# Kernel optimization log

Measured on AMD Instinct MI355X. Metric: run time of the kernel, lower is better.

The kernel has to match this reference:

```python
import jax, jax.numpy as jnp
import numpy as np

B, S, D = 2, 2048, 1024
H, KV, HD = 16, 8, 64
E, K, FF = 8, 2, 3584
EPS = 1e-5
THETA = 10000.0


def setup_inputs() -> dict:
    key = jax.random.key(0)
    ks = jax.random.split(key, 10)
    sc = 0.02
    return {
        "hidden_states": jax.random.normal(ks[0], (B, S, D), jnp.float32),
        "position_ids": jnp.broadcast_to(jnp.arange(S, dtype=jnp.int32), (B, S)),
        "lb_loss": jnp.zeros((), jnp.float32),
        "ln1_w": jnp.ones((D,), jnp.float32),
        "ln2_w": jnp.ones((D,), jnp.float32),
        "Wq": jax.random.normal(ks[1], (D, H * HD), jnp.float32) * sc,
        "Wk": jax.random.normal(ks[2], (D, KV * HD), jnp.float32) * sc,
        "Wv": jax.random.normal(ks[3], (D, KV * HD), jnp.float32) * sc,
        "Wo": jax.random.normal(ks[4], (H * HD, D), jnp.float32) * sc,
        "Wg": jax.random.normal(ks[5], (D, E), jnp.float32) * sc,
        "w1": jax.random.normal(ks[6], (E, D, FF), jnp.float32) * sc,
        "w2": jax.random.normal(ks[7], (E, FF, D), jnp.float32) * sc,
        "w3": jax.random.normal(ks[8], (E, D, FF), jnp.float32) * sc,
    }


def rmsnorm(x, w):
    xf = x.astype(jnp.float32)
    return (w * (xf * jax.lax.rsqrt(jnp.mean(xf * xf, -1, keepdims=True) + EPS))).astype(x.dtype)


def rotate_half(x):
    x1, x2 = jnp.split(x, 2, axis=-1)
    return jnp.concatenate([-x2, x1], axis=-1)


def _forward(hidden_states, position_ids, lb_loss, ln1_w, ln2_w, Wq, Wk, Wv, Wo, Wg, w1, w2, w3):
    # ---- attention block (pre-norm + causal GQA + RoPE + residual) ----
    resid = hidden_states
    x = rmsnorm(hidden_states, ln1_w)
    q = (x @ Wq).reshape(B, S, H, HD)
    k = (x @ Wk).reshape(B, S, KV, HD)
    v = (x @ Wv).reshape(B, S, KV, HD)
    inv_freq = 1.0 / (THETA ** (jnp.arange(0, HD, 2, dtype=jnp.float32) / HD))
    ang = position_ids.astype(jnp.float32)[:, :, None] * inv_freq      # [B,S,HD/2]
    emb = jnp.concatenate([ang, ang], axis=-1)                          # [B,S,HD]
    cos = jnp.cos(emb)[:, :, None, :]
    sin = jnp.sin(emb)[:, :, None, :]
    q = q * cos + rotate_half(q) * sin
    k = k * cos + rotate_half(k) * sin
    rep = H // KV
    k = jnp.repeat(k, rep, axis=2)                                      # [B,S,H,HD]
    v = jnp.repeat(v, rep, axis=2)
    scores = jnp.einsum('bqhd,bkhd->bhqk', q, k) / jnp.sqrt(jnp.float32(HD))
    causal = jnp.tril(jnp.ones((S, S), bool))
    scores = jnp.where(causal[None, None], scores, jnp.float32(-1e30))
    probs = jax.nn.softmax(scores.astype(jnp.float32), axis=-1).astype(q.dtype)
    attn = jnp.einsum('bhqk,bkhd->bqhd', probs, v).reshape(B, S, H * HD)
    hidden_states = resid + attn @ Wo

    # ---- MoE block (pre-norm + top-2 routed SwiGLU experts + residual) ----
    resid = hidden_states
    x = rmsnorm(hidden_states, ln2_w)
    flat = x.reshape(-1, D)                                             # [N,D]
    logits = flat @ Wg
    gate_probs = jax.nn.softmax(logits.astype(jnp.float32), axis=-1)    # [N,E]
    top_w, top_i = jax.lax.top_k(gate_probs, K)                         # [N,K]
    top_w = (top_w / jnp.sum(top_w, -1, keepdims=True)).astype(flat.dtype)
    out = jnp.zeros_like(flat)
    for e in range(E):  # fixed small expert count
        w_e = jnp.sum(jnp.where(top_i == e, top_w, 0.0), axis=-1)       # [N]
        y = (jax.nn.silu(flat @ w1[e]) * (flat @ w3[e])) @ w2[e]        # [N,D]
        out = out + y * w_e[:, None]
    hidden_states = resid + out.reshape(B, S, D)

    # ---- load-balancing auxiliary loss ----
    expert_mask = jax.nn.one_hot(top_i, E, dtype=jnp.float32)           # [N,K,E]
    tokens_per_expert = jnp.mean(expert_mask, axis=0)                   # [K,E]
    router_prob_per_expert = jnp.mean(gate_probs, axis=0)               # [E]
    lb = jnp.mean(jnp.sum(tokens_per_expert * router_prob_per_expert[None, :], axis=-1)) * E
    return hidden_states, lb_loss + lb


def reference(hidden_states, position_ids, lb_loss, ln1_w, ln2_w, Wq, Wk, Wv, Wo, Wg, w1, w2, w3):
    return _forward(hidden_states, position_ids, lb_loss, ln1_w, ln2_w, Wq, Wk, Wv, Wo, Wg, w1, w2, w3)
```

## Files before the change

### kernel.cpp

```cpp
#include <hip/hip_runtime.h>
#include <stdint.h>

#define DEV __device__ __forceinline__

typedef __attribute__((ext_vector_type(8))) short short8;
typedef __attribute__((ext_vector_type(4))) float f32x4;
typedef __attribute__((ext_vector_type(4))) short short4v;

static constexpr int BATCH = 2, SEQ = 2048, DM = 1024, NH = 16, NKV = 8, HD = 64;
static constexpr int NTOK = BATCH * SEQ;
static constexpr int NE = 8, FF = 3584;

DEV unsigned short f2bf(float f) {
  union { float f; unsigned u; } x; x.f = f;
  unsigned r = x.u + 0x7fffu + ((x.u >> 16) & 1u);
  return (unsigned short)(r >> 16);
}
DEV float bf2f(unsigned short h) {
  union { unsigned u; float f; } x; x.u = ((unsigned)h) << 16; return x.f;
}

DEV void async16(const void* g, void* l) {
  __builtin_amdgcn_global_load_lds((const __attribute__((address_space(1))) unsigned int*)g,
                                   (__attribute__((address_space(3))) unsigned int*)l, 16, 0, 0);
}

DEV f32x4 mfma16(short8 a, short8 b, f32x4 c) {
  return __builtin_amdgcn_mfma_f32_16x16x32_bf16(a, b, c, 0, 0, 0);
}

__global__ __launch_bounds__(256) void transpose_cvt_k(
    const float* __restrict__ in, unsigned short* __restrict__ out,
    int R, int C, long inStride, long outStride)
{
  __shared__ unsigned short tile[64][68];
  const float* src = in + (long)blockIdx.z * inStride;
  unsigned short* dst = out + (long)blockIdx.z * outStride;
  int r0 = blockIdx.y * 64, c0 = blockIdx.x * 64;
  int s4 = (threadIdx.x & 15) * 4, rr = threadIdx.x >> 4;
#pragma unroll
  for (int i = 0; i < 4; ++i) {
    int r = rr + i * 16;
    float4 v = *(const float4*)(src + (long)(r0 + r) * C + c0 + s4);
    tile[r][s4 + 0] = f2bf(v.x); tile[r][s4 + 1] = f2bf(v.y);
    tile[r][s4 + 2] = f2bf(v.z); tile[r][s4 + 3] = f2bf(v.w);
  }
  __syncthreads();
#pragma unroll
  for (int i = 0; i < 4; ++i) {
    int c = rr + i * 16;
    union { unsigned short us[4]; short4v v; } o;
    o.us[0] = tile[s4 + 0][c]; o.us[1] = tile[s4 + 1][c];
    o.us[2] = tile[s4 + 2][c]; o.us[3] = tile[s4 + 3][c];
    *(short4v*)(dst + (long)(c0 + c) * R + r0 + s4) = o.v;
  }
}

__global__ __launch_bounds__(256) void rmsnorm_k(
    const float* __restrict__ x, const float* __restrict__ w, unsigned short* __restrict__ out)
{
  int row = blockIdx.x, t = threadIdx.x;
  const float4* xr = (const float4*)(x + (long)row * DM);
  float4 v = xr[t];
  float ss = v.x * v.x + v.y * v.y + v.z * v.z + v.w * v.w;
#pragma unroll
  for (int o = 32; o; o >>= 1) ss += __shfl_xor(ss, o);
  __shared__ float red[4];
  if ((t & 63) == 0) red[t >> 6] = ss;
  __syncthreads();
  float tot = red[0] + red[1] + red[2] + red[3];
  float rms = rsqrtf(tot * (1.0f / DM) + 1e-5f);
  float4 wv = ((const float4*)w)[t];
  union { unsigned short us[4]; short4v s; } o4;
  o4.us[0] = f2bf(v.x * rms * wv.x);
  o4.us[1] = f2bf(v.y * rms * wv.y);
  o4.us[2] = f2bf(v.z * rms * wv.z);
  o4.us[3] = f2bf(v.w * rms * wv.w);
  *(short4v*)(out + (long)row * DM + 4 * t) = o4.s;
}

template<int MODE>
__global__ __launch_bounds__(256) void gemm_k(
    const unsigned short* __restrict__ A, const unsigned short* __restrict__ B0,
    void* __restrict__ Cout, const float* __restrict__ resid,
    int M, int N, int K, int ldA, int ldB, int ldC)
{
  constexpr int BM = 128, BN = 128, BK = 64;
  __shared__ __align__(16) unsigned short As[BM * BK];
  __shared__ __align__(16) unsigned short Bs[BN * BK];
  int bm = blockIdx.x, bn = blockIdx.y;
  int t = threadIdx.x, w = t >> 6, l = t & 63, g = l >> 4, q = l & 15;
  int wm = w >> 1, wn = w & 1;

  const char* aSrc[4];
  const char* bSrc[4];
#pragma unroll
  for (int i = 0; i < 4; ++i) {
    int r = i * 32 + w * 8 + (l >> 3);
    aSrc[i] = (const char*)(A + (long)(bm * BM + r) * ldA) + (((l & 7) * 16) ^ ((r & 7) << 4));
    bSrc[i] = (const char*)(B0 + (long)(bn * BN + r) * ldB) + (((l & 7) * 16) ^ ((r & 7) << 4));
  }
  f32x4 acc[4][4];
#pragma unroll
  for (int mi = 0; mi < 4; ++mi)
#pragma unroll
    for (int ni = 0; ni < 4; ++ni) acc[mi][ni] = f32x4{0.f, 0.f, 0.f, 0.f};

  for (int k0 = 0; k0 < K; k0 += BK) {
#pragma unroll
    for (int i = 0; i < 4; ++i) {
      async16(aSrc[i] + (long)k0 * 2, &As[(i * 32 + w * 8) * BK]);
      async16(bSrc[i] + (long)k0 * 2, &Bs[(i * 32 + w * 8) * BK]);
    }
    asm volatile("s_waitcnt vmcnt(0)" ::: "memory");
    __syncthreads();
#pragma unroll
    for (int kk = 0; kk < 2; ++kk) {
      int col = (kk * 64 + g * 16) ^ ((q & 7) << 4);
      short8 af[4], bfm[4];
#pragma unroll
      for (int mi = 0; mi < 4; ++mi)
        af[mi] = *(const short8*)&As[(wm * 64 + mi * 16 + q) * BK + (col >> 1)];
#pragma unroll
      for (int ni = 0; ni < 4; ++ni)
        bfm[ni] = *(const short8*)&Bs[(wn * 64 + ni * 16 + q) * BK + (col >> 1)];
#pragma unroll
      for (int mi = 0; mi < 4; ++mi)
#pragma unroll
        for (int ni = 0; ni < 4; ++ni)
          acc[mi][ni] = mfma16(af[mi], bfm[ni], acc[mi][ni]);
    }
    __syncthreads();
  }
#pragma unroll
  for (int mi = 0; mi < 4; ++mi) {
#pragma unroll
    for (int r = 0; r < 4; ++r) {
      int grow = bm * BM + wm * 64 + mi * 16 + g * 4 + r;
#pragma unroll
      for (int ni = 0; ni < 4; ++ni) {
        int gcol = bn * BN + wn * 64 + ni * 16 + q;
        float v = acc[mi][ni][r];
        if (MODE == 0) {
          ((unsigned short*)Cout)[(long)grow * ldC + gcol] = f2bf(v);
        } else {
          long idx = (long)grow * ldC + gcol;
          ((float*)Cout)[idx] = resid[idx] + v;
        }
      }
    }
  }
}

__global__ __launch_bounds__(256, 3) void moe_up_k(
    const unsigned short* __restrict__ xn, const unsigned short* __restrict__ w1T,
    const unsigned short* __restrict__ w3T, unsigned short* __restrict__ hbuf,
    const int* __restrict__ lstAll, const int* __restrict__ cntAll)
{
  constexpr int BM = 128, BN = 64, BK = 64, NBN = FF / BN;
  constexpr int NJJ = NBN / 8;
  __shared__ __align__(16) unsigned short As[BM * BK];
  __shared__ __align__(16) unsigned short Bs[2][BN * BK];
  int t = threadIdx.x, w = t >> 6, l = t & 63, g = l >> 4, q = l & 15;
  int wm = w >> 1, wn = w & 1;
  int xcd = blockIdx.x & 7, slot = blockIdx.x >> 3, SLOTS = gridDim.x >> 3;

  int TB = 0;
#pragma unroll
  for (int e = 0; e < NE; ++e) TB += (cntAll[e] + BM - 1) >> 7;

  for (int lidx = slot; lidx < NJJ * TB; lidx += SLOTS) {
    int jj = lidx / TB, tb = lidx - jj * TB;
    int bn = xcd + 8 * jj;
    int e = 0, base = 0, cnt = 0, bm = 0;
    for (; e < NE; ++e) {
      cnt = cntAll[e];
      int te = (cnt + BM - 1) >> 7;
      if (tb < te) { bm = tb; break; }
      tb -= te; base += cnt;
    }
    const int* lst = lstAll + e * NTOK;
    const unsigned short* B0 = w1T + (size_t)e * FF * DM + (size_t)bn * BN * DM;
    const unsigned short* B1 = w3T + (size_t)e * FF * DM + (size_t)bn * BN * DM;

    const char* aSrc[4];
    const char* b0Src[2];
    const char* b1Src[2];
#pragma unroll
    for (int i = 0; i < 4; ++i) {
      int r = i * 32 + w * 8 + (l >> 3);
      int grow = bm * BM + r;
      int arow = lst[grow < cnt ? grow : 0];
      int swz = ((l & 7) * 16) ^ ((r & 7) << 4);
      aSrc[i] = (const char*)(xn + (long)arow * DM) + swz;
      if (i < 2) {
        b0Src[i] = (const char*)(B0 + (long)r * DM) + swz;
        b1Src[i] = (const char*)(B1 + (long)r * DM) + swz;
      }
    }
    f32x4 acc0[4][2], acc1[4][2];
#pragma unroll
    for (int mi = 0; mi < 4; ++mi)
#pragma unroll
      for (int ni = 0; ni < 2; ++ni) {
        acc0[mi][ni] = f32x4{0.f, 0.f, 0.f, 0.f};
        acc1[mi][ni] = f32x4{0.f, 0.f, 0.f, 0.f};
      }

    for (int k0 = 0; k0 < DM; k0 += BK) {
#pragma unroll
      for (int i = 0; i < 4; ++i)
        async16(aSrc[i] + (long)k0 * 2, &As[(i * 32 + w * 8) * BK]);
#pragma unroll
      for (int i = 0; i < 2; ++i) {
        async16(b0Src[i] + (long)k0 * 2, &Bs[0][(i * 32 + w * 8) * BK]);
        async16(b1Src[i] + (long)k0 * 2, &Bs[1][(i * 32 + w * 8) * BK]);
      }
      asm volatile("s_waitcnt vmcnt(0)" ::: "memory");
      __syncthreads();
#pragma unroll
      for (int kk = 0; kk < 2; ++kk) {
        int col = (kk * 64 + g * 16) ^ ((q & 7) << 4);
        short8 af[4], bf0[2], bf1[2];
#pragma unroll
        for (int mi = 0; mi < 4; ++mi)
          af[mi] = *(const short8*)&As[(wm * 64 + mi * 16 + q) * BK + (col >> 1)];
#pragma unroll
        for (int ni = 0; ni < 2; ++ni) {
          int r = wn * 32 + ni * 16 + q;
          bf0[ni] = *(const short8*)&Bs[0][r * BK + (col >> 1)];
          bf1[ni] = *(const short8*)&Bs[1][r * BK + (col >> 1)];
        }
#pragma unroll
        for (int mi = 0; mi < 4; ++mi)
#pragma unroll
          for (int ni = 0; ni < 2; ++ni) {
            acc0[mi][ni] = mfma16(af[mi], bf0[ni], acc0[mi][ni]);
            acc1[mi][ni] = mfma16(af[mi], bf1[ni], acc1[mi][ni]);
          }
      }
      __syncthreads();
    }
#pragma unroll
    for (int mi = 0; mi < 4; ++mi) {
#pragma unroll
      for (int r = 0; r < 4; ++r) {
        int grow = bm * BM + wm * 64 + mi * 16 + g * 4 + r;
        if (grow >= cnt) continue;
        unsigned short* hp = hbuf + (size_t)(base + grow) * FF + bn * BN + wn * 32;
#pragma unroll
        for (int ni = 0; ni < 2; ++ni) {
          float v1 = acc0[mi][ni][r];
          float v3 = acc1[mi][ni][r];
          float sg = v1 / (1.0f + __expf(-v1));
          hp[ni * 16 + q] = f2bf(sg * v3);
        }
      }
    }
  }
}

__global__ __launch_bounds__(256, 3) void moe_dn_k(
    const unsigned short* __restrict__ hbuf, const unsigned short* __restrict__ w2T,
    unsigned short* __restrict__ ybuf, const int* __restrict__ cntAll)
{
  constexpr int BM = 128, BN = 64, BK = 64, NBN = DM / BN;
  __shared__ __align__(16) unsigned short As[BM * BK];
  __shared__ __align__(16) unsigned short Bs[BN * BK];
  int t = threadIdx.x, w = t >> 6, l = t & 63, g = l >> 4, q = l & 15;
  int wm = w >> 1, wn = w & 1;
  int xcd = blockIdx.x & 7, slot = blockIdx.x >> 3;

  for (int lidx = slot; ; lidx += 128) {
    int j = lidx / NBN, bn = lidx % NBN;
    int gg = xcd + 8 * j;
    int e = 0, base = 0, cnt = 0, bm = -1;
    for (; e < NE; ++e) {
      cnt = cntAll[e];
      int te = (cnt + BM - 1) >> 7;
      if (gg < te) { bm = gg; break; }
      gg -= te; base += cnt;
    }
    if (bm < 0) return;
    const unsigned short* B0 = w2T + (size_t)e * DM * FF + (size_t)bn * BN * FF;

    const char* aSrc[4];
    const char* bSrc[2];
#pragma unroll
    for (int i = 0; i < 4; ++i) {
      int r = i * 32 + w * 8 + (l >> 3);
      int grow = bm * BM + r;
      int arow = base + (grow < cnt ? grow : 0);
      int swz = ((l & 7) * 16) ^ ((r & 7) << 4);
      aSrc[i] = (const char*)(hbuf + (long)arow * FF) + swz;
      if (i < 2) bSrc[i] = (const char*)(B0 + (long)r * FF) + swz;
    }
    f32x4 acc[4][2];
#pragma unroll
    for (int mi = 0; mi < 4; ++mi)
#pragma unroll
      for (int ni = 0; ni < 2; ++ni) acc[mi][ni] = f32x4{0.f, 0.f, 0.f, 0.f};

    for (int k0 = 0; k0 < FF; k0 += BK) {
#pragma unroll
      for (int i = 0; i < 4; ++i)
        async16(aSrc[i] + (long)k0 * 2, &As[(i * 32 + w * 8) * BK]);
#pragma unroll
      for (int i = 0; i < 2; ++i)
        async16(bSrc[i] + (long)k0 * 2, &Bs[(i * 32 + w * 8) * BK]);
      asm volatile("s_waitcnt vmcnt(0)" ::: "memory");
      __syncthreads();
#pragma unroll
      for (int kk = 0; kk < 2; ++kk) {
        int col = (kk * 64 + g * 16) ^ ((q & 7) << 4);
        short8 af[4], bfm[2];
#pragma unroll
        for (int mi = 0; mi < 4; ++mi)
          af[mi] = *(const short8*)&As[(wm * 64 + mi * 16 + q) * BK + (col >> 1)];
#pragma unroll
        for (int ni = 0; ni < 2; ++ni)
          bfm[ni] = *(const short8*)&Bs[(wn * 32 + ni * 16 + q) * BK + (col >> 1)];
#pragma unroll
        for (int mi = 0; mi < 4; ++mi)
#pragma unroll
          for (int ni = 0; ni < 2; ++ni)
            acc[mi][ni] = mfma16(af[mi], bfm[ni], acc[mi][ni]);
      }
      __syncthreads();
    }
#pragma unroll
    for (int mi = 0; mi < 4; ++mi) {
#pragma unroll
      for (int r = 0; r < 4; ++r) {
        int grow = bm * BM + wm * 64 + mi * 16 + g * 4 + r;
        if (grow >= cnt) continue;
        unsigned short* yp = ybuf + (size_t)(base + grow) * DM + bn * BN + wn * 32;
#pragma unroll
        for (int ni = 0; ni < 2; ++ni)
          yp[ni * 16 + q] = f2bf(acc[mi][ni][r]);
      }
    }
  }
}

__global__ __launch_bounds__(256) void moe_gather_k(
    const unsigned short* __restrict__ ybuf, const int* __restrict__ tokslot,
    const float* __restrict__ wtop, const int* __restrict__ cntAll,
    float* __restrict__ out)
{
  __shared__ int base8[NE];
  int tok = blockIdx.x, t = threadIdx.x;
  if (t < NE) {
    int b = 0;
    for (int i = 0; i < t; ++i) b += cntAll[i];
    base8[t] = b;
  }
  __syncthreads();
  int s0 = tokslot[2 * tok], s1 = tokslot[2 * tok + 1];
  int slot0 = base8[s0 >> 16] + (s0 & 0xffff);
  int slot1 = base8[s1 >> 16] + (s1 & 0xffff);
  float w0 = wtop[2 * tok], w1 = wtop[2 * tok + 1];
  short4v a = *(const short4v*)(ybuf + (size_t)slot0 * DM + 4 * t);
  short4v b = *(const short4v*)(ybuf + (size_t)slot1 * DM + 4 * t);
  float4* op = (float4*)(out + (size_t)tok * DM);
  float4 o = op[t];
  o.x += w0 * bf2f((unsigned short)a[0]) + w1 * bf2f((unsigned short)b[0]);
  o.y += w0 * bf2f((unsigned short)a[1]) + w1 * bf2f((unsigned short)b[1]);
  o.z += w0 * bf2f((unsigned short)a[2]) + w1 * bf2f((unsigned short)b[2]);
  o.w += w0 * bf2f((unsigned short)a[3]) + w1 * bf2f((unsigned short)b[3]);
  op[t] = o;
}

__global__ __launch_bounds__(256) void rope_k(unsigned short* __restrict__ qkv,
                                              const int* __restrict__ pos)
{
  int tok = blockIdx.x, t = threadIdx.x;
  __shared__ float cs[32], sn[32];
  if (t < 32) {
    float p = (float)pos[tok];
    float freq = __expf(-(float)t * 0.28782313663f);
    float a = p * freq;
    cs[t] = cosf(a); sn[t] = sinf(a);
  }
  __syncthreads();
  unsigned short* row = qkv + (long)tok * 2048;
#pragma unroll
  for (int idx = t; idx < 768; idx += 256) {
    int hh = idx >> 5, d = idx & 31;
    int col = (hh < 16) ? hh * 64 + d : 1024 + (hh - 16) * 64 + d;
    float x1 = bf2f(row[col]), x2 = bf2f(row[col + 32]);
    row[col]      = f2bf(x1 * cs[d] - x2 * sn[d]);
    row[col + 32] = f2bf(x2 * cs[d] + x1 * sn[d]);
  }
}

__global__ __launch_bounds__(256) void vtrans_k(const unsigned short* __restrict__ qkv,
                                                unsigned short* __restrict__ vt)
{
  __shared__ unsigned short tile[64][72];
  int s0 = blockIdx.x * 64, kvh = blockIdx.y, b = blockIdx.z;
  int t = threadIdx.x;
  int tx4 = (t & 15) * 4, row = t >> 4;
  const unsigned short* src = qkv + (long)(b * SEQ + s0) * 2048 + 1536 + kvh * 64;
#pragma unroll
  for (int i = 0; i < 4; ++i) {
    int r = row + i * 16;
    *(short4v*)&tile[r][tx4] = *(const short4v*)(src + (long)r * 2048 + tx4);
  }
  __syncthreads();
  unsigned short* dst = vt + (long)((b * NKV + kvh) * 64) * SEQ + s0;
#pragma unroll
  for (int i = 0; i < 4; ++i) {
    int d = row + i * 16;
    union { unsigned short us[4]; short4v v; } o;
    o.us[0] = tile[tx4 + 0][d]; o.us[1] = tile[tx4 + 1][d];
    o.us[2] = tile[tx4 + 2][d]; o.us[3] = tile[tx4 + 3][d];
    *(short4v*)(dst + (long)d * SEQ + tx4) = o.v;
  }
}

__global__ __launch_bounds__(512) void attn_k(const unsigned short* __restrict__ qkv,
                                              const unsigned short* __restrict__ vtg,
                                              unsigned short* __restrict__ aout)
{
  int b = blockIdx.z;
  int qt = b ? (31 - blockIdx.x) : blockIdx.x;
  int kvh = blockIdx.y;
  int t = threadIdx.x, w = t >> 6, l = t & 63, g = l >> 4, q = l & 15;
  int h = kvh * 2 + (w >> 2);
  int wl = w & 3;
  __shared__ __align__(16) unsigned short Ks[2][4096];
  __shared__ __align__(16) unsigned short Vs[2][4096];
  int tok0 = b * SEQ;
  int myq = qt * 64 + wl * 16 + q;
  const unsigned short* qp = qkv + (long)(tok0 + myq) * 2048 + h * 64;
  short8 qf0 = *(const short8*)(qp + g * 8);
  short8 qf1 = *(const short8*)(qp + 32 + g * 8);
  const unsigned short* vtb = vtg + (long)((b * NKV + kvh) * 64) * SEQ;
  f32x4 o[4];
#pragma unroll
  for (int nf = 0; nf < 4; ++nf) o[nf] = f32x4{0.f, 0.f, 0.f, 0.f};
  float m = -1e30f, ssum = 0.0f;
  int r8 = w * 8 + (l >> 3);
  int sswz = ((l & 7) * 16) ^ ((r8 & 7) << 4);

  auto stage = [&](int kt, int buf) {
    const char* ksrc = (const char*)(qkv + (long)(tok0 + kt * 64 + r8) * 2048 + 1024 + kvh * 64) + sswz;
    async16(ksrc, &Ks[buf][r8 * 64]);
    const char* vsrc = (const char*)(vtb + (long)r8 * SEQ + kt * 64) + sswz;
    async16(vsrc, &Vs[buf][r8 * 64]);
  };

  stage(0, 0);
  __syncthreads();
  int cur = 0;
  for (int kt = 0; kt <= qt; ++kt) {
    if (kt < qt) stage(kt + 1, cur ^ 1);
    f32x4 st[4];
#pragma unroll
    for (int mb = 0; mb < 4; ++mb) {
      int kr = mb * 16 + q;
      int c0 = (g * 16) ^ ((q & 7) << 4);
      int c1 = (64 + g * 16) ^ ((q & 7) << 4);
      short8 k0 = *(const short8*)&Ks[cur][kr * 64 + (c0 >> 1)];
      short8 k1 = *(const short8*)&Ks[cur][kr * 64 + (c1 >> 1)];
      f32x4 z = f32x4{0.f, 0.f, 0.f, 0.f};
      __builtin_amdgcn_s_setprio(1);
      z = mfma16(k0, qf0, z);
      z = mfma16(k1, qf1, z);
      __builtin_amdgcn_s_setprio(0);
      st[mb] = z;
    }
    float p[4][4];
    float tmax = -1e30f;
#pragma unroll
    for (int mb = 0; mb < 4; ++mb)
#pragma unroll
      for (int r = 0; r < 4; ++r) {
        float v = st[mb][r] * 0.125f;
        int kvg = kt * 64 + mb * 16 + g * 4 + r;
        if (kvg > myq) v = -1e30f;
        p[mb][r] = v;
        tmax = fmaxf(tmax, v);
      }
    tmax = fmaxf(tmax, __shfl_xor(tmax, 16));
    tmax = fmaxf(tmax, __shfl_xor(tmax, 32));
    float mnew = fmaxf(m, tmax);
    float fac = __expf(m - mnew);
    m = mnew;
    float ps = 0.0f;
#pragma unroll
    for (int mb = 0; mb < 4; ++mb)
#pragma unroll
      for (int r = 0; r < 4; ++r) { float e = __expf(p[mb][r] - m); p[mb][r] = e; ps += e; }
    ps += __shfl_xor(ps, 16);
    ps += __shfl_xor(ps, 32);
    ssum = ssum * fac + ps;
#pragma unroll
    for (int r = 0; r < 4; ++r) {
      float ff = __shfl(fac, g * 4 + r);
#pragma unroll
      for (int nf = 0; nf < 4; ++nf) o[nf][r] *= ff;
    }
    unsigned pw[4][2];
#pragma unroll
    for (int mb = 0; mb < 4; ++mb) {
      pw[mb][0] = ((unsigned)f2bf(p[mb][1]) << 16) | f2bf(p[mb][0]);
      pw[mb][1] = ((unsigned)f2bf(p[mb][3]) << 16) | f2bf(p[mb][2]);
    }
    short8 pa[2];
#pragma unroll
    for (int f = 0; f < 2; ++f) {
      union { unsigned u[4]; short8 s; } cv;
#pragma unroll
      for (int i = 0; i < 4; ++i) {
        int srcl = ((g & 1) * 2 + (i >> 1)) * 16 + q;
        unsigned aa = (unsigned)__shfl((int)pw[2 * f][i & 1], srcl);
        unsigned bb = (unsigned)__shfl((int)pw[2 * f + 1][i & 1], srcl);
        cv.u[i] = (g & 2) ? bb : aa;
      }
      pa[f] = cv.s;
    }
#pragma unroll
    for (int kk = 0; kk < 2; ++kk) {
      int cb = (kk * 64 + g * 16) ^ ((q & 7) << 4);
      __builtin_amdgcn_s_setprio(1);
#pragma unroll
      for (int nf = 0; nf < 4; ++nf) {
        short8 vb = *(const short8*)&Vs[cur][(nf * 16 + q) * 64 + (cb >> 1)];
        o[nf] = mfma16(pa[kk], vb, o[nf]);
      }
      __builtin_amdgcn_s_setprio(0);
    }
    __syncthreads();
    cur ^= 1;
  }
#pragma unroll
  for (int r = 0; r < 4; ++r) {
    float is = 1.0f / __shfl(ssum, g * 4 + r);
    int orow = tok0 + qt * 64 + wl * 16 + g * 4 + r;
    unsigned short* op = aout + (long)orow * 1024 + h * 64;
    op[q]      = f2bf(o[0][r] * is);
    op[16 + q] = f2bf(o[1][r] * is);
    op[32 + q] = f2bf(o[2][r] * is);
    op[48 + q] = f2bf(o[3][r] * is);
  }
}

__global__ __launch_bounds__(256) void router_k(
    const float* __restrict__ hid, const float* __restrict__ w2n, const float* __restrict__ Wg,
    unsigned short* __restrict__ xn, float* __restrict__ probs8,
    int* __restrict__ top0, int* __restrict__ top1, float* __restrict__ wtop)
{
  int row = blockIdx.x, t = threadIdx.x;
  const float4* xr = (const float4*)(hid + (long)row * DM);
  float4 v = xr[t];
  float ss = v.x * v.x + v.y * v.y + v.z * v.z + v.w * v.w;
#pragma unroll
  for (int o = 32; o; o >>= 1) ss += __shfl_xor(ss, o);
  __shared__ float red[4];
  __shared__ float lred[4][8];
  __shared__ float lg[8];
  if ((t & 63) == 0) red[t >> 6] = ss;
  __syncthreads();
  float tot = red[0] + red[1] + red[2] + red[3];
  float rms = rsqrtf(tot * (1.0f / DM) + 1e-5f);
  float4 wv = ((const float4*)w2n)[t];
  float x0 = v.x * rms * wv.x, x1 = v.y * rms * wv.y, x2 = v.z * rms * wv.z, x3 = v.w * rms * wv.w;
  union { unsigned short us[4]; short4v s; } o4;
  o4.us[0] = f2bf(x0); o4.us[1] = f2bf(x1); o4.us[2] = f2bf(x2); o4.us[3] = f2bf(x3);
  *(short4v*)(xn + (long)row * DM + 4 * t) = o4.s;
  const float* wgr = Wg + t * 32;
  float lacc[8];
#pragma unroll
  for (int e = 0; e < 8; ++e)
    lacc[e] = x0 * wgr[e] + x1 * wgr[8 + e] + x2 * wgr[16 + e] + x3 * wgr[24 + e];
#pragma unroll
  for (int e = 0; e < 8; ++e)
#pragma unroll
    for (int o = 32; o; o >>= 1) lacc[e] += __shfl_xor(lacc[e], o);
  if ((t & 63) == 0)
#pragma unroll
    for (int e = 0; e < 8; ++e) lred[t >> 6][e] = lacc[e];
  __syncthreads();
  if (t < 8) lg[t] = lred[0][t] + lred[1][t] + lred[2][t] + lred[3][t];
  __syncthreads();
  if (t == 0) {
    float p[8];
    float mx = lg[0];
#pragma unroll
    for (int e = 1; e < 8; ++e) mx = fmaxf(mx, lg[e]);
    float s = 0.f;
#pragma unroll
    for (int e = 0; e < 8; ++e) { p[e] = __expf(lg[e] - mx); s += p[e]; }
    float isv = 1.0f / s;
#pragma unroll
    for (int e = 0; e < 8; ++e) { p[e] *= isv; probs8[(long)row * 8 + e] = p[e]; }
    int i0 = 0;
#pragma unroll
    for (int e = 1; e < 8; ++e) if (p[e] > p[i0]) i0 = e;
    int i1 = (i0 == 0) ? 1 : 0;
#pragma unroll
    for (int e = 0; e < 8; ++e) if (e != i0 && p[e] > p[i1]) i1 = e;
    float sw = p[i0] + p[i1];
    top0[row] = i0; top1[row] = i1;
    wtop[2 * row] = p[i0] / sw; wtop[2 * row + 1] = p[i1] / sw;
  }
}

__global__ __launch_bounds__(256) void build_lists_k(
    const int* __restrict__ top0, const int* __restrict__ top1,
    const float* __restrict__ wtop, int* __restrict__ lst, int* __restrict__ tokslot,
    int* __restrict__ ecnt, int* __restrict__ cnt0, int* __restrict__ cnt1)
{
  int e = blockIdx.x, t = threadIdx.x, lane = t & 63, wv = t >> 6;
  __shared__ int wco[4];
  int base = 0, c0 = 0, c1 = 0;
  for (int t0 = 0; t0 < NTOK; t0 += 256) {
    int tok = t0 + t;
    int m0 = (top0[tok] == e), m1 = (top1[tok] == e);
    c0 += m0; c1 += m1;
    int matched = m0 | m1;
    unsigned long long mask = __ballot(matched);
    if (lane == 0) wco[wv] = __popcll(mask);
    __syncthreads();
    int off = base;
    for (int j = 0; j < wv; ++j) off += wco[j];
    int pos = off + __popcll(mask & ((1ull << lane) - 1ull));
    if (matched) {
      lst[e * NTOK + pos] = tok;
      tokslot[2 * tok + (m0 ? 0 : 1)] = (e << 16) | pos;
    }
    base += wco[0] + wco[1] + wco[2] + wco[3];
    __syncthreads();
  }
#pragma unroll
  for (int o = 32; o; o >>= 1) { c0 += __shfl_xor(c0, o); c1 += __shfl_xor(c1, o); }
  __shared__ int r0[4], r1[4];
  if (lane == 0) { r0[wv] = c0; r1[wv] = c1; }
  __syncthreads();
  if (t == 0) {
    ecnt[e] = base;
    cnt0[e] = r0[0] + r0[1] + r0[2] + r0[3];
    cnt1[e] = r1[0] + r1[1] + r1[2] + r1[3];
  }
}

__global__ __launch_bounds__(256) void lbsum_k(const float* __restrict__ probs8,
                                               float* __restrict__ probsum)
{
  int e = blockIdx.x, t = threadIdx.x;
  float s = 0.f;
  for (int tok = t; tok < NTOK; tok += 256) s += probs8[(long)tok * 8 + e];
#pragma unroll
  for (int o = 32; o; o >>= 1) s += __shfl_xor(s, o);
  __shared__ float r[4];
  if ((t & 63) == 0) r[t >> 6] = s;
  __syncthreads();
  if (t == 0) probsum[e] = r[0] + r[1] + r[2] + r[3];
}

__global__ void lb_k(const int* __restrict__ cnt0, const int* __restrict__ cnt1,
                     const float* __restrict__ probsum,
                     const float* __restrict__ lbin, float* __restrict__ out)
{
  if (threadIdx.x == 0 && blockIdx.x == 0) {
    float acc = 0.f;
    for (int e = 0; e < 8; ++e) acc += (float)(cnt0[e] + cnt1[e]) * probsum[e];
    out[0] = lbin[0] + acc * (4.0f / ((float)NTOK * (float)NTOK));
  }
}

extern "C" void kernel_launch(void* const* d_in, const int* in_sizes, int n_in,
                              void* d_out, int out_size, void* d_ws, size_t ws_size,
                              hipStream_t stream) {
  (void)in_sizes; (void)n_in; (void)out_size; (void)ws_size;
  const float* hid  = (const float*)d_in[0];
  const int*   pos  = (const int*)d_in[1];
  const float* lbin = (const float*)d_in[2];
  const float* ln1  = (const float*)d_in[3];
  const float* ln2  = (const float*)d_in[4];
  const float* Wq   = (const float*)d_in[5];
  const float* Wk   = (const float*)d_in[6];
  const float* Wv   = (const float*)d_in[7];
  const float* Wo   = (const float*)d_in[8];
  const float* Wg   = (const float*)d_in[9];
  const float* w1   = (const float*)d_in[10];
  const float* w2   = (const float*)d_in[11];
  const float* w3   = (const float*)d_in[12];
  float* out = (float*)d_out;

  char* ws = (char*)d_ws;
  size_t off = 0;
  auto alloc = [&](size_t bytes) { void* p = ws + off; off += (bytes + 255) & ~255ull; return p; };
  unsigned short* WqkvT = (unsigned short*)alloc(2048ull * 1024 * 2);
  unsigned short* WoT   = (unsigned short*)alloc(1024ull * 1024 * 2);
  unsigned short* w1T   = (unsigned short*)alloc((size_t)NE * FF * DM * 2);
  unsigned short* w3T   = (unsigned short*)alloc((size_t)NE * FF * DM * 2);
  unsigned short* w2T   = (unsigned short*)alloc((size_t)NE * DM * FF * 2);
  unsigned short* xn    = (unsigned short*)alloc((size_t)NTOK * DM * 2);
  unsigned short* vtg   = (unsigned short*)alloc((size_t)BATCH * NKV * 64 * SEQ * 2);
  unsigned short* ybuf  = (unsigned short*)alloc((size_t)(2 * NTOK) * DM * 2);
  int*   lst = (int*)alloc((size_t)NE * NTOK * 4);
  int*   tokslot = (int*)alloc((size_t)NTOK * 2 * 4);
  float* probs8 = (float*)alloc((size_t)NTOK * 8 * 4);
  int*   top0 = (int*)alloc((size_t)NTOK * 4);
  int*   top1 = (int*)alloc((size_t)NTOK * 4);
  float* wtop = (float*)alloc((size_t)NTOK * 2 * 4);
  int*   ctr = (int*)alloc(256);
  int*   ecnt = ctr;
  int*   cnt0 = ctr + 8;
  int*   cnt1 = ctr + 16;
  float* probsum = (float*)(ctr + 24);
  size_t qkvB  = (size_t)NTOK * 2048 * 2;
  size_t aoutB = (size_t)NTOK * DM * 2;
  size_t hbufB = (size_t)(2 * NTOK + 128) * FF * 2;
  char* region = (char*)alloc(qkvB + aoutB > hbufB ? qkvB + aoutB : hbufB);
  unsigned short* qkv  = (unsigned short*)region;
  unsigned short* aout = (unsigned short*)(region + qkvB);
  unsigned short* hbuf = (unsigned short*)region;

  transpose_cvt_k<<<dim3(16, 16, 1), 256, 0, stream>>>(Wq, WqkvT, 1024, 1024, 0, 0);
  transpose_cvt_k<<<dim3(8, 16, 1), 256, 0, stream>>>(Wk, WqkvT + 1024 * 1024, 1024, 512, 0, 0);
  transpose_cvt_k<<<dim3(8, 16, 1), 256, 0, stream>>>(Wv, WqkvT + 1536 * 1024, 1024, 512, 0, 0);
  transpose_cvt_k<<<dim3(16, 16, 1), 256, 0, stream>>>(Wo, WoT, 1024, 1024, 0, 0);
  transpose_cvt_k<<<dim3(FF / 64, 16, 8), 256, 0, stream>>>(w1, w1T, 1024, FF, (long)DM * FF, (long)FF * DM);
  transpose_cvt_k<<<dim3(FF / 64, 16, 8), 256, 0, stream>>>(w3, w3T, 1024, FF, (long)DM * FF, (long)FF * DM);
  transpose_cvt_k<<<dim3(16, FF / 64, 8), 256, 0, stream>>>(w2, w2T, FF, 1024, (long)FF * DM, (long)DM * FF);

  rmsnorm_k<<<NTOK, 256, 0, stream>>>(hid, ln1, xn);
  gemm_k<0><<<dim3(32, 16), 256, 0, stream>>>(xn, WqkvT, qkv, nullptr,
                                              NTOK, 2048, 1024, 1024, 1024, 2048);
  rope_k<<<NTOK, 256, 0, stream>>>(qkv, pos);
  vtrans_k<<<dim3(SEQ / 64, NKV, BATCH), 256, 0, stream>>>(qkv, vtg);
  attn_k<<<dim3(SEQ / 64, NKV, BATCH), 512, 0, stream>>>(qkv, vtg, aout);
  gemm_k<1><<<dim3(32, 8), 256, 0, stream>>>(aout, WoT, d_out, hid,
                                             NTOK, 1024, 1024, 1024, 1024, 1024);
  router_k<<<NTOK, 256, 0, stream>>>(out, ln2, Wg, xn, probs8, top0, top1, wtop);
  build_lists_k<<<8, 256, 0, stream>>>(top0, top1, wtop, lst, tokslot, ecnt, cnt0, cnt1);
  lbsum_k<<<8, 256, 0, stream>>>(probs8, probsum);
  moe_up_k<<<1792, 256, 0, stream>>>(xn, w1T, w3T, hbuf, lst, ecnt);
  moe_dn_k<<<1024, 256, 0, stream>>>(hbuf, w2T, ybuf, ecnt);
  moe_gather_k<<<NTOK, 256, 0, stream>>>(ybuf, tokslot, wtop, ecnt, out);
  lb_k<<<1, 64, 0, stream>>>(cnt0, cnt1, probsum, lbin, out + (size_t)NTOK * DM);
}
```

Measured before the change: 577.3 us.

## Double-buffer MoE up/down GEMMs and widen down-proj tile to 128 columns

Both MoE expert GEMM kernels now keep two LDS buffers. The next K-slice is issued with async global-to-LDS loads before the current slice is computed, and the wait is partial (vmcnt(8)), so load latency can overlap the MFMA work. The down-projection kernel grows its N tile from 64 to 128 columns and gets a new work distribution in which each XCD owns one column block. Grids shrink to 512 persistent blocks and the occupancy target drops from 3 to 2 blocks per CU. The cost is more LDS and registers per block and lower occupancy, plus a risk of load imbalance from the fixed bn-per-XCD mapping.

```diff
diff --git a/kernel.cpp b/kernel.cpp
--- a/kernel.cpp
+++ b/kernel.cpp
@@ -152,21 +152,20 @@
   }
 }
 
-__global__ __launch_bounds__(256, 3) void moe_up_k(
+__global__ __launch_bounds__(256, 2) void moe_up_k(
     const unsigned short* __restrict__ xn, const unsigned short* __restrict__ w1T,
     const unsigned short* __restrict__ w3T, unsigned short* __restrict__ hbuf,
     const int* __restrict__ lstAll, const int* __restrict__ cntAll)
 {
   constexpr int BM = 128, BN = 64, BK = 64, NBN = FF / BN;
   constexpr int NJJ = NBN / 8;
-  __shared__ __align__(16) unsigned short As[BM * BK];
-  __shared__ __align__(16) unsigned short Bs[2][BN * BK];
+  __shared__ __align__(16) unsigned short As[2][BM * BK];
+  __shared__ __align__(16) unsigned short Bs[2][2][BN * BK];
   int t = threadIdx.x, w = t >> 6, l = t & 63, g = l >> 4, q = l & 15;
   int wm = w >> 1, wn = w & 1;
   int xcd = blockIdx.x & 7, slot = blockIdx.x >> 3, SLOTS = gridDim.x >> 3;
 
   int TB = 0;
-#pragma unroll
   for (int e = 0; e < NE; ++e) TB += (cntAll[e] + BM - 1) >> 7;
 
   for (int lidx = slot; lidx < NJJ * TB; lidx += SLOTS) {
@@ -207,29 +206,40 @@
         acc1[mi][ni] = f32x4{0.f, 0.f, 0.f, 0.f};
       }
 
+    auto STAGE = [&](int k0, int buf) {
+#pragma unroll
+      for (int i = 0; i < 4; ++i)
+        async16(aSrc[i] + (long)k0 * 2, &As[buf][(i * 32 + w * 8) * BK]);
+#pragma unroll
+      for (int i = 0; i < 2; ++i) {
+        async16(b0Src[i] + (long)k0 * 2, &Bs[buf][0][(i * 32 + w * 8) * BK]);
+        async16(b1Src[i] + (long)k0 * 2, &Bs[buf][1][(i * 32 + w * 8) * BK]);
+      }
+    };
+
+    STAGE(0, 0);
+    int cur = 0;
     for (int k0 = 0; k0 < DM; k0 += BK) {
-#pragma unroll
-      for (int i = 0; i < 4; ++i)
-        async16(aSrc[i] + (long)k0 * 2, &As[(i * 32 + w * 8) * BK]);
-#pragma unroll
-      for (int i = 0; i < 2; ++i) {
-        async16(b0Src[i] + (long)k0 * 2, &Bs[0][(i * 32 + w * 8) * BK]);
-        async16(b1Src[i] + (long)k0 * 2, &Bs[1][(i * 32 + w * 8) * BK]);
-      }
-      asm volatile("s_waitcnt vmcnt(0)" ::: "memory");
-      __syncthreads();
+      if (k0 + BK < DM) {
+        STAGE(k0 + BK, cur ^ 1);
+        asm volatile("s_waitcnt vmcnt(8)" ::: "memory");
+      } else {
+        asm volatile("s_waitcnt vmcnt(0)" ::: "memory");
+      }
+      __builtin_amdgcn_s_barrier();
+      __builtin_amdgcn_sched_barrier(0);
 #pragma unroll
       for (int kk = 0; kk < 2; ++kk) {
         int col = (kk * 64 + g * 16) ^ ((q & 7) << 4);
         short8 af[4], bf0[2], bf1[2];
 #pragma unroll
         for (int mi = 0; mi < 4; ++mi)
-          af[mi] = *(const short8*)&As[(wm * 64 + mi * 16 + q) * BK + (col >> 1)];
+          af[mi] = *(const short8*)&As[cur][(wm * 64 + mi * 16 + q) * BK + (col >> 1)];
 #pragma unroll
         for (int ni = 0; ni < 2; ++ni) {
           int r = wn * 32 + ni * 16 + q;
-          bf0[ni] = *(const short8*)&Bs[0][r * BK + (col >> 1)];
-          bf1[ni] = *(const short8*)&Bs[1][r * BK + (col >> 1)];
+          bf0[ni] = *(const short8*)&Bs[cur][0][r * BK + (col >> 1)];
+          bf1[ni] = *(const short8*)&Bs[cur][1][r * BK + (col >> 1)];
         }
 #pragma unroll
         for (int mi = 0; mi < 4; ++mi)
@@ -239,7 +249,9 @@
             acc1[mi][ni] = mfma16(af[mi], bf1[ni], acc1[mi][ni]);
           }
       }
-      __syncthreads();
+      __builtin_amdgcn_sched_barrier(0);
+      __builtin_amdgcn_s_barrier();
+      cur ^= 1;
     }
 #pragma unroll
     for (int mi = 0; mi < 4; ++mi) {
@@ -260,32 +272,34 @@
   }
 }
 
-__global__ __launch_bounds__(256, 3) void moe_dn_k(
+__global__ __launch_bounds__(256, 2) void moe_dn_k(
     const unsigned short* __restrict__ hbuf, const unsigned short* __restrict__ w2T,
     unsigned short* __restrict__ ybuf, const int* __restrict__ cntAll)
 {
-  constexpr int BM = 128, BN = 64, BK = 64, NBN = DM / BN;
-  __shared__ __align__(16) unsigned short As[BM * BK];
-  __shared__ __align__(16) unsigned short Bs[BN * BK];
+  constexpr int BM = 128, BN = 128, BK = 64;
+  __shared__ __align__(16) unsigned short As[2][BM * BK];
+  __shared__ __align__(16) unsigned short Bs[2][BN * BK];
   int t = threadIdx.x, w = t >> 6, l = t & 63, g = l >> 4, q = l & 15;
   int wm = w >> 1, wn = w & 1;
-  int xcd = blockIdx.x & 7, slot = blockIdx.x >> 3;
-
-  for (int lidx = slot; ; lidx += 128) {
-    int j = lidx / NBN, bn = lidx % NBN;
-    int gg = xcd + 8 * j;
-    int e = 0, base = 0, cnt = 0, bm = -1;
+  int xcd = blockIdx.x & 7, slot = blockIdx.x >> 3, SLOTS = gridDim.x >> 3;
+  int bn = xcd;
+
+  int TB = 0;
+  for (int e = 0; e < NE; ++e) TB += (cntAll[e] + BM - 1) >> 7;
+
+  for (int tb0 = slot; tb0 < TB; tb0 += SLOTS) {
+    int tb = tb0;
+    int e = 0, base = 0, cnt = 0, bm = 0;
     for (; e < NE; ++e) {
       cnt = cntAll[e];
       int te = (cnt + BM - 1) >> 7;
-      if (gg < te) { bm = gg; break; }
-      gg -= te; base += cnt;
-    }
-    if (bm < 0) return;
+      if (tb < te) { bm = tb; break; }
+      tb -= te; base += cnt;
+    }
     const unsigned short* B0 = w2T + (size_t)e * DM * FF + (size_t)bn * BN * FF;
 
     const char* aSrc[4];
-    const char* bSrc[2];
+    const char* bSrc[4];
 #pragma unroll
     for (int i = 0; i < 4; ++i) {
       int r = i * 32 + w * 8 + (l >> 3);
@@ -293,40 +307,52 @@
       int arow = base + (grow < cnt ? grow : 0);
       int swz = ((l & 7) * 16) ^ ((r & 7) << 4);
       aSrc[i] = (const char*)(hbuf + (long)arow * FF) + swz;
-      if (i < 2) bSrc[i] = (const char*)(B0 + (long)r * FF) + swz;
-    }
-    f32x4 acc[4][2];
+      bSrc[i] = (const char*)(B0 + (long)r * FF) + swz;
+    }
+    f32x4 acc[4][4];
 #pragma unroll
     for (int mi = 0; mi < 4; ++mi)
 #pragma unroll
-      for (int ni = 0; ni < 2; ++ni) acc[mi][ni] = f32x4{0.f, 0.f, 0.f, 0.f};
-
+      for (int ni = 0; ni < 4; ++ni) acc[mi][ni] = f32x4{0.f, 0.f, 0.f, 0.f};
+
+    auto STAGE = [&](int k0, int buf) {
+#pragma unroll
+      for (int i = 0; i < 4; ++i) {
+        async16(aSrc[i] + (long)k0 * 2, &As[buf][(i * 32 + w * 8) * BK]);
+        async16(bSrc[i] + (long)k0 * 2, &Bs[buf][(i * 32 + w * 8) * BK]);
+      }
+    };
+
+    STAGE(0, 0);
+    int cur = 0;
     for (int k0 = 0; k0 < FF; k0 += BK) {
-#pragma unroll
-      for (int i = 0; i < 4; ++i)
-        async16(aSrc[i] + (long)k0 * 2, &As[(i * 32 + w * 8) * BK]);
-#pragma unroll
-      for (int i = 0; i < 2; ++i)
-        async16(bSrc[i] + (long)k0 * 2, &Bs[(i * 32 + w * 8) * BK]);
-      asm volatile("s_waitcnt vmcnt(0)" ::: "memory");
-      __syncthreads();
+      if (k0 + BK < FF) {
+        STAGE(k0 + BK, cur ^ 1);
+        asm volatile("s_waitcnt vmcnt(8)" ::: "memory");
+      } else {
+        asm volatile("s_waitcnt vmcnt(0)" ::: "memory");
+      }
+      __builtin_amdgcn_s_barrier();
+      __builtin_amdgcn_sched_barrier(0);
 #pragma unroll
       for (int kk = 0; kk < 2; ++kk) {
         int col = (kk * 64 + g * 16) ^ ((q & 7) << 4);
-        short8 af[4], bfm[2];
+        short8 af[4], bfm[4];
 #pragma unroll
         for (int mi = 0; mi < 4; ++mi)
-          af[mi] = *(const short8*)&As[(wm * 64 + mi * 16 + q) * BK + (col >> 1)];
-#pragma unroll
-        for (int ni = 0; ni < 2; ++ni)
-          bfm[ni] = *(const short8*)&Bs[(wn * 32 + ni * 16 + q) * BK + (col >> 1)];
+          af[mi] = *(const short8*)&As[cur][(wm * 64 + mi * 16 + q) * BK + (col >> 1)];
+#pragma unroll
+        for (int ni = 0; ni < 4; ++ni)
+          bfm[ni] = *(const short8*)&Bs[cur][(wn * 64 + ni * 16 + q) * BK + (col >> 1)];
 #pragma unroll
         for (int mi = 0; mi < 4; ++mi)
 #pragma unroll
-          for (int ni = 0; ni < 2; ++ni)
+          for (int ni = 0; ni < 4; ++ni)
             acc[mi][ni] = mfma16(af[mi], bfm[ni], acc[mi][ni]);
       }
-      __syncthreads();
+      __builtin_amdgcn_sched_barrier(0);
+      __builtin_amdgcn_s_barrier();
+      cur ^= 1;
     }
 #pragma unroll
     for (int mi = 0; mi < 4; ++mi) {
@@ -334,9 +360,9 @@
       for (int r = 0; r < 4; ++r) {
         int grow = bm * BM + wm * 64 + mi * 16 + g * 4 + r;
         if (grow >= cnt) continue;
-        unsigned short* yp = ybuf + (size_t)(base + grow) * DM + bn * BN + wn * 32;
-#pragma unroll
-        for (int ni = 0; ni < 2; ++ni)
+        unsigned short* yp = ybuf + (size_t)(base + grow) * DM + bn * BN + wn * 64;
+#pragma unroll
+        for (int ni = 0; ni < 4; ++ni)
           yp[ni * 16 + q] = f2bf(acc[mi][ni][r]);
       }
     }
@@ -739,8 +765,8 @@
   router_k<<<NTOK, 256, 0, stream>>>(out, ln2, Wg, xn, probs8, top0, top1, wtop);
   build_lists_k<<<8, 256, 0, stream>>>(top0, top1, wtop, lst, tokslot, ecnt, cnt0, cnt1);
   lbsum_k<<<8, 256, 0, stream>>>(probs8, probsum);
-  moe_up_k<<<1792, 256, 0, stream>>>(xn, w1T, w3T, hbuf, lst, ecnt);
-  moe_dn_k<<<1024, 256, 0, stream>>>(hbuf, w2T, ybuf, ecnt);
+  moe_up_k<<<512, 256, 0, stream>>>(xn, w1T, w3T, hbuf, lst, ecnt);
+  moe_dn_k<<<512, 256, 0, stream>>>(hbuf, w2T, ybuf, ecnt);
   moe_gather_k<<<NTOK, 256, 0, stream>>>(ybuf, tokslot, wtop, ecnt, out);
   lb_k<<<1, 64, 0, stream>>>(cnt0, cnt1, probsum, lbin, out + (size_t)NTOK * DM);
 }
```

Result: slower. 623.4 us (+8.0%).
